# Performance work log

Measured on AMD Instinct MI355X. Metric: run time of the kernel, lower is better.

Reference implementation:

```python
import jax, jax.numpy as jnp
import numpy as np

B, C, H, D, W = 1, 32, 32, 32, 32   # batch, channels, 3D grid
M1 = M2 = M3 = 16                   # fourier modes kept per dim
KS = 3                              # spatial attention kernel size
MEM = 5                             # memory slots
EPS = 1e-5
N = H * D * W


def _gelu(x):
    return jax.nn.gelu(x, approximate=False)  # torch exact GELU


def _gn(x):
    # GroupNorm(1, C) without affine: normalize over (C,H,D,W) per sample
    mu = jnp.mean(x, axis=(1, 2, 3, 4), keepdims=True)
    var = jnp.var(x, axis=(1, 2, 3, 4), keepdims=True)
    return (x - mu) * jax.lax.rsqrt(var + EPS)


def _spectral_conv(x, wr, wi):
    # classic 3D FNO spectral conv: keep low modes (4 corner blocks in dims H,D; low block in rfft dim W)
    xf = jnp.fft.rfftn(x, axes=(2, 3, 4))                 # (B,C,H,D,W//2+1) complex64
    w = wr + 1j * wi                                      # (4,Cin,Cout,M1,M2,M3)
    of = jnp.zeros((x.shape[0], C, H, D, W // 2 + 1), xf.dtype)
    corners = [(slice(0, M1), slice(0, M2)), (slice(H - M1, H), slice(0, M2)),
               (slice(0, M1), slice(D - M2, D)), (slice(H - M1, H), slice(D - M2, D))]
    for i, (s1, s2) in enumerate(corners):
        of = of.at[:, :, s1, s2, :M3].set(
            jnp.einsum('bixyz,ioxyz->boxyz', xf[:, :, s1, s2, :M3], w[i]))
    return jnp.fft.irfftn(of, s=(H, D, W), axes=(2, 3, 4))


def _forward(x, t, prev_memory, w_spec_r, w_spec_i, norm1_g, norm1_b,
             mlp_w1, mlp_b1, mlp_w2, mlp_b2, tin_gw, tin_gb, tin_bw, tin_bb,
             q_w, q_b, k_w, k_b, v_w, v_b, mem_key, mem_value,
             gate_w, gate_b, gru_wih, gru_whh, gru_bih, gru_bhh):
    skip1 = x
    skip2 = _gelu(x)
    # spectral conv -> GroupNorm(affine) + residual -> gelu
    h = _spectral_conv(x, w_spec_r, w_spec_i)
    h = _gelu(_gn(h) * norm1_g[None, :, None, None, None]
              + norm1_b[None, :, None, None, None] + skip1)
    # pointwise Conv1d MLP over channels
    hf = h.reshape(B, C, N)
    u = _gelu(jnp.einsum('oc,bcn->bon', mlp_w1, hf) + mlp_b1[None, :, None])
    hf = jnp.einsum('oc,bcn->bon', mlp_w2, u) + mlp_b2[None, :, None]
    h = hf.reshape(B, C, H, D, W)
    # time-conditioned instance norm: gamma/beta from 1x1 conv over t (B,C)
    gamma = (jnp.einsum('oc,bc->bo', tin_gw, t) + tin_gb)[:, :, None, None, None]
    beta = (jnp.einsum('oc,bc->bo', tin_bw, t) + tin_bb)[:, :, None, None, None]
    h = gamma * _gn(h) + beta
    # ---- spatial attention with memory ----
    pad = KS // 2
    xp = jnp.pad(h, ((0, 0), (0, 0), (pad, pad), (pad, pad), (pad, pad)))
    # 3D unfold: (B,C,27,N) patches via 27 shifted views
    patches = jnp.stack([xp[:, :, i:i + H, j:j + D, l:l + W]
                         for i in range(KS) for j in range(KS) for l in range(KS)],
                        axis=2).reshape(B, C, KS ** 3, N)
    hf = h.reshape(B, C, N)
    q = jnp.einsum('oc,bcn->bon', q_w, hf) + q_b[None, :, None]              # (B,C,N)
    k_sp = jnp.einsum('oc,bcmn->bomn', k_w, patches) + k_b[None, :, None, None]
    v_sp = jnp.einsum('oc,bcmn->bomn', v_w, patches) + v_b[None, :, None, None]
    mem_k = jnp.broadcast_to(mem_key[None, :, :, None], (B, C, MEM, N))
    mem_v = jnp.broadcast_to(mem_value[None, :, :, None], (B, C, MEM, N))
    k = jnp.concatenate([mem_k, k_sp], axis=2)                               # (B,C,32,N)
    v = jnp.concatenate([mem_v, v_sp], axis=2)
    attn = jax.nn.softmax(q[:, :, None, :] * k / jnp.sqrt(jnp.float32(C)), axis=2)
    out = jnp.sum(attn * v, axis=2)                                          # (B,C,N)
    cat = jnp.concatenate([hf, out], axis=1)                                 # (B,2C,N)
    gate = jax.nn.sigmoid(jnp.einsum('oc,bcn->bon', gate_w, cat) + gate_b[None, :, None])
    out = gate * out + (1.0 - gate) * hf
    out = out.reshape(B, C, H, D, W)
    # GRUCell memory update from spatially pooled features
    m_in = jnp.mean(out, axis=(2, 3, 4))                                     # (B,C)
    gi = m_in @ gru_wih.T + gru_bih
    gh = prev_memory @ gru_whh.T + gru_bhh
    ir, iz, inn = jnp.split(gi, 3, axis=1)
    hr, hz, hn = jnp.split(gh, 3, axis=1)
    r = jax.nn.sigmoid(ir + hr)
    z = jax.nn.sigmoid(iz + hz)
    n = jnp.tanh(inn + r * hn)
    new_memory = (1.0 - z) * n + z * prev_memory                             # (B,C)
    return out + skip2, new_memory


def setup_inputs():
    key = jax.random.key(0)
    ks = jax.random.split(key, 20)
    def rn(k, shape, s):
        return jax.random.normal(k, shape, jnp.float32) * s
    spec_scale = 1.0 / (C * C)
    return dict(
        x=jax.random.normal(ks[0], (B, C, H, D, W), jnp.float32),
        t=jax.random.normal(ks[1], (B, C), jnp.float32),
        prev_memory=jnp.zeros((B, C), jnp.float32),
        w_spec_r=rn(ks[2], (4, C, C, M1, M2, M3), spec_scale),
        w_spec_i=rn(ks[3], (4, C, C, M1, M2, M3), spec_scale),
        norm1_g=jnp.ones((C,), jnp.float32),
        norm1_b=jnp.zeros((C,), jnp.float32),
        mlp_w1=rn(ks[4], (C // 2, C), 0.1), mlp_b1=jnp.zeros((C // 2,), jnp.float32),
        mlp_w2=rn(ks[5], (C, C // 2), 0.1), mlp_b2=jnp.zeros((C,), jnp.float32),
        tin_gw=rn(ks[6], (C, C), 0.1), tin_gb=jnp.ones((C,), jnp.float32),
        tin_bw=rn(ks[7], (C, C), 0.1), tin_bb=jnp.zeros((C,), jnp.float32),
        q_w=rn(ks[8], (C, C), 0.1), q_b=jnp.zeros((C,), jnp.float32),
        k_w=rn(ks[9], (C, C), 0.1), k_b=jnp.zeros((C,), jnp.float32),
        v_w=rn(ks[10], (C, C), 0.1), v_b=jnp.zeros((C,), jnp.float32),
        mem_key=jax.random.normal(ks[11], (C, MEM), jnp.float32),
        mem_value=jax.random.normal(ks[12], (C, MEM), jnp.float32),
        gate_w=rn(ks[13], (C, 2 * C), 0.1), gate_b=jnp.zeros((C,), jnp.float32),
        gru_wih=rn(ks[14], (3 * C, C), 0.1), gru_whh=rn(ks[15], (3 * C, C), 0.1),
        gru_bih=jnp.zeros((3 * C,), jnp.float32), gru_bhh=jnp.zeros((3 * C,), jnp.float32),
    )


def reference(x, t, prev_memory, w_spec_r, w_spec_i, norm1_g, norm1_b,
              mlp_w1, mlp_b1, mlp_w2, mlp_b2, tin_gw, tin_gb, tin_bw, tin_bb,
              q_w, q_b, k_w, k_b, v_w, v_b, mem_key, mem_value,
              gate_w, gate_b, gru_wih, gru_whh, gru_bih, gru_bhh):
    return _forward(x, t, prev_memory, w_spec_r, w_spec_i, norm1_g, norm1_b,
                    mlp_w1, mlp_b1, mlp_w2, mlp_b2, tin_gw, tin_gb, tin_bw, tin_bb,
                    q_w, q_b, k_w, k_b, v_w, v_b, mem_key, mem_value,
                    gate_w, gate_b, gru_wih, gru_whh, gru_bih, gru_bhh)
```

## Files before the change

### kernel.cpp

```cpp
#include <hip/hip_runtime.h>
#include <hip/hip_bf16.h>
#include <math.h>

#define NSP 32768
#define NZ 17

typedef float f4_t __attribute__((ext_vector_type(4)));

__device__ __forceinline__ float geluf(float x){
    return 0.5f * x * (1.0f + erff(x * 0.70710678118654752f));
}
__device__ __forceinline__ float sigmoidf_(float x){
    return 1.0f / (1.0f + __expf(-x));
}


__global__ void k_fwd(const float* __restrict__ x, float* __restrict__ Br, float* __restrict__ Bi){
    __shared__ float tile[32*33];
    __shared__ float ar[544], ai[544];
    __shared__ float ct[32], st[32];
    int b = blockIdx.x, t = threadIdx.x;
    if (t < 32){ float ang = 6.283185307179586477f * (float)t / 32.0f; ct[t] = cosf(ang); st[t] = sinf(ang); }
    const float* src = x + b * 1024;
    for (int j = t; j < 1024; j += 256) tile[(j & 31) * 33 + (j >> 5)] = src[j];
    __syncthreads();
    for (int idx = t; idx < 544; idx += 256){
        int d = idx / 17, z = idx - d * 17;
        float sr = 0.f, si = 0.f;
        #pragma unroll
        for (int w = 0; w < 32; ++w){
            int a = (z * w) & 31;
            float v = tile[w * 33 + d];
            sr += v * ct[a];
            si -= v * st[a];
        }
        ar[idx] = sr; ai[idx] = si;
    }
    __syncthreads();
    for (int idx = t; idx < 544; idx += 256){
        int kd = idx / 17, z = idx - kd * 17;
        float sr = 0.f, si = 0.f;
        #pragma unroll
        for (int d = 0; d < 32; ++d){
            int a = (kd * d) & 31;
            float c = ct[a], s = st[a];
            float vr = ar[d * 17 + z], vi = ai[d * 17 + z];
            sr += vr * c + vi * s;
            si += vi * c - vr * s;
        }
        Br[b * 544 + idx] = sr; Bi[b * 544 + idx] = si;
    }
}

__global__ void k_fft_h(const float* __restrict__ Br, const float* __restrict__ Bi,
                        float* __restrict__ Ar, float* __restrict__ Ai){
    __shared__ float ir[544], ii[544];
    __shared__ float ct[32], st[32];
    int b = blockIdx.x, t = threadIdx.x;
    int c = b >> 5, d = b & 31;
    if (t < 32){ float ang = 6.283185307179586477f * (float)t / 32.0f; ct[t] = cosf(ang); st[t] = sinf(ang); }
    for (int j = t; j < 544; j += 256){
        int h = j / 17, z = j - h * 17;
        int g = ((c * 32 + h) * 32 + d) * NZ + z;
        ir[j] = Br[g]; ii[j] = Bi[g];
    }
    __syncthreads();
    for (int idx = t; idx < 544; idx += 256){
        int kh = idx / 17, z = idx - kh * 17;
        float sr = 0.f, si = 0.f;
        #pragma unroll
        for (int h = 0; h < 32; ++h){
            int a = (kh * h) & 31;
            float c2 = ct[a], s2 = st[a];
            float vr = ir[h * 17 + z], vi = ii[h * 17 + z];
            sr += vr * c2 + vi * s2;
            si += vi * c2 - vr * s2;
        }
        int g = ((c * 32 + kh) * 32 + d) * NZ + z;
        Ar[g] = sr; Ai[g] = si;
    }
}

__global__ void k_modemul(const float* __restrict__ Xr, const float* __restrict__ Xi,
                          const float* __restrict__ Wr, const float* __restrict__ Wi,
                          float* __restrict__ Or, float* __restrict__ Oi){
    int b = blockIdx.x;
    int q = b & 3;
    int o = (b >> 2) & 31;
    int corner = b >> 7;
    int t = threadIdx.x;
    int m = q * 1024 + t * 4;
    int xm = m >> 8, ym = (m >> 4) & 15, zm = m & 15;
    int xg = xm + ((corner & 1) << 4);
    int y  = ym + ((corner >> 1) << 4);
    if (t < 128){
        int xl = t >> 5;
        int arr = (t >> 4) & 1;
        int yl = t & 15;
        int xgz = q * 4 + xl + ((corner & 1) << 4);
        int yz = yl + ((corner >> 1) << 4);
        int g = ((o * 32 + xgz) * 32 + yz) * NZ + 16;
        if (arr == 0) Or[g] = 0.f; else Oi[g] = 0.f;
    }
    size_t xoff = (size_t)(xg * 32 + y) * NZ + zm;
    const float* wr = Wr + (size_t)((corner * 32) * 32 + o) * 4096 + m;
    const float* wi = Wi + (size_t)((corner * 32) * 32 + o) * 4096 + m;
    float ar0=0.f, ar1=0.f, ar2=0.f, ar3=0.f;
    float ai0=0.f, ai1=0.f, ai2=0.f, ai3=0.f;
    #pragma unroll 4
    for (int i = 0; i < 32; ++i){
        f4_t w4r = __builtin_nontemporal_load((const f4_t*)(wr + (size_t)i * 131072));
        f4_t w4i = __builtin_nontemporal_load((const f4_t*)(wi + (size_t)i * 131072));
        const float* pxr = Xr + (size_t)i * 17408 + xoff;
        const float* pxi = Xi + (size_t)i * 17408 + xoff;
        float xr0 = pxr[0], xr1 = pxr[1], xr2 = pxr[2], xr3 = pxr[3];
        float xi0 = pxi[0], xi1 = pxi[1], xi2 = pxi[2], xi3 = pxi[3];
        ar0 += w4r.x * xr0 - w4i.x * xi0;  ai0 += w4r.x * xi0 + w4i.x * xr0;
        ar1 += w4r.y * xr1 - w4i.y * xi1;  ai1 += w4r.y * xi1 + w4i.y * xr1;
        ar2 += w4r.z * xr2 - w4i.z * xi2;  ai2 += w4r.z * xi2 + w4i.z * xr2;
        ar3 += w4r.w * xr3 - w4i.w * xi3;  ai3 += w4r.w * xi3 + w4i.w * xr3;
    }
    int g = ((o * 32 + xg) * 32 + y) * NZ + zm;
    Or[g + 0] = ar0; Or[g + 1] = ar1; Or[g + 2] = ar2; Or[g + 3] = ar3;
    Oi[g + 0] = ai0; Oi[g + 1] = ai1; Oi[g + 2] = ai2; Oi[g + 3] = ai3;
}

__global__ void k_ifft_h(const float* __restrict__ Br, const float* __restrict__ Bi,
                         float* __restrict__ Ar, float* __restrict__ Ai){
    __shared__ float ir[544], ii[544];
    __shared__ float ct[32], st[32];
    int b = blockIdx.x, t = threadIdx.x;
    int c = b >> 5, y = b & 31;
    if (t < 32){ float ang = 6.283185307179586477f * (float)t / 32.0f; ct[t] = cosf(ang); st[t] = sinf(ang); }
    for (int j = t; j < 544; j += 256){
        int xk = j / 17, z = j - xk * 17;
        int g = ((c * 32 + xk) * 32 + y) * NZ + z;
        ir[j] = Br[g]; ii[j] = Bi[g];
    }
    __syncthreads();
    for (int idx = t; idx < 544; idx += 256){
        int h = idx / 17, z = idx - h * 17;
        float sr = 0.f, si = 0.f;
        #pragma unroll
        for (int k = 0; k < 32; ++k){
            int a = (k * h) & 31;
            float c2 = ct[a], s2 = st[a];
            float vr = ir[k * 17 + z], vi = ii[k * 17 + z];
            sr += vr * c2 - vi * s2;
            si += vr * s2 + vi * c2;
        }
        int g = ((c * 32 + h) * 32 + y) * NZ + z;
        Ar[g] = sr; Ai[g] = si;
    }
}

__global__ void k_inv(const float* __restrict__ Ar, const float* __restrict__ Ai,
                      float* __restrict__ spec,
                      float* __restrict__ psum, float* __restrict__ psq){
    __shared__ float ir[544], ii[544];
    __shared__ float cr[544], ci[544];
    __shared__ float ct[32], st[32];
    __shared__ float ls[256], lq[256];
    int b = blockIdx.x, t = threadIdx.x;
    if (t < 32){ float ang = 6.283185307179586477f * (float)t / 32.0f; ct[t] = cosf(ang); st[t] = sinf(ang); }
    const float* pr = Ar + b * 544;
    const float* pi = Ai + b * 544;
    for (int j = t; j < 544; j += 256){ ir[j] = pr[j]; ii[j] = pi[j]; }
    __syncthreads();
    for (int idx = t; idx < 544; idx += 256){
        int d = idx / 17, z = idx - d * 17;
        float sr = 0.f, si = 0.f;
        #pragma unroll
        for (int k = 0; k < 32; ++k){
            int a = (k * d) & 31;
            float c2 = ct[a], s2 = st[a];
            float vr = ir[k * 17 + z], vi = ii[k * 17 + z];
            sr += vr * c2 - vi * s2;
            si += vr * s2 + vi * c2;
        }
        cr[idx] = sr; ci[idx] = si;
    }
    __syncthreads();
    const float inv = 1.0f / 32768.0f;
    float s_loc = 0.f, q_loc = 0.f;
    for (int idx = t; idx < 1024; idx += 256){
        int d = idx >> 5, w = idx & 31;
        float s = cr[d * 17 + 0] + ((w & 1) ? -cr[d * 17 + 16] : cr[d * 17 + 16]);
        #pragma unroll
        for (int z = 1; z < 16; ++z){
            int a = (z * w) & 31;
            s += 2.0f * (cr[d * 17 + z] * ct[a] - ci[d * 17 + z] * st[a]);
        }
        s *= inv;
        spec[b * 1024 + idx] = s;
        s_loc += s; q_loc += s * s;
    }
    ls[t] = s_loc; lq[t] = q_loc; __syncthreads();
    for (int off = 128; off > 0; off >>= 1){
        if (t < off){ ls[t] += ls[t + off]; lq[t] += lq[t + off]; }
        __syncthreads();
    }
    if (t == 0){ psum[b] = ls[0]; psq[b] = lq[0]; }
}


__global__ void k_mlp(const float* __restrict__ spec, const float* __restrict__ x,
                      const float* __restrict__ n1g, const float* __restrict__ n1b,
                      const float* __restrict__ psum, const float* __restrict__ psq,
                      const float* __restrict__ w1, const float* __restrict__ b1,
                      const float* __restrict__ w2, const float* __restrict__ b2,
                      float* __restrict__ h2,
                      float* __restrict__ psum2, float* __restrict__ psq2){
    __shared__ float W1[512], W2[512], B1[16], B2[32], GG[32], BB[32];
    __shared__ float ls[256], lq[256];
    int t = threadIdx.x;
    for (int j = t; j < 512; j += 256){ W1[j] = w1[j]; W2[j] = w2[j]; }
    if (t < 16) B1[t] = b1[t];
    if (t < 32){ B2[t] = b2[t]; GG[t] = n1g[t]; BB[t] = n1b[t]; }
    float s0 = 0.f, q0 = 0.f;
    for (int j = t; j < 1024; j += 256){ s0 += psum[j]; q0 += psq[j]; }
    ls[t] = s0; lq[t] = q0; __syncthreads();
    for (int off = 128; off > 0; off >>= 1){
        if (t < off){ ls[t] += ls[t + off]; lq[t] += lq[t + off]; }
        __syncthreads();
    }
    float mu = ls[0] * (1.0f / 1048576.0f);
    float var = lq[0] * (1.0f / 1048576.0f) - mu * mu;
    float rs = rsqrtf(var + 1e-5f);
    __syncthreads();
    int n = blockIdx.x * 256 + t;
    float hv[32];
    #pragma unroll
    for (int c = 0; c < 32; ++c){
        float v = (spec[c * NSP + n] - mu) * rs * GG[c] + BB[c] + x[c * NSP + n];
        hv[c] = geluf(v);
    }
    float u[16];
    #pragma unroll
    for (int o = 0; o < 16; ++o){
        float a = B1[o];
        #pragma unroll
        for (int c = 0; c < 32; ++c) a += W1[o * 32 + c] * hv[c];
        u[o] = geluf(a);
    }
    float s_loc = 0.f, q_loc = 0.f;
    #pragma unroll
    for (int o = 0; o < 32; ++o){
        float a = B2[o];
        #pragma unroll
        for (int c = 0; c < 16; ++c) a += W2[o * 16 + c] * u[c];
        h2[o * NSP + n] = a;
        s_loc += a; q_loc += a * a;
    }
    ls[t] = s_loc; lq[t] = q_loc; __syncthreads();
    for (int off = 128; off > 0; off >>= 1){
        if (t < off){ ls[t] += ls[t + off]; lq[t] += lq[t + off]; }
        __syncthreads();
    }
    if (t == 0){ psum2[blockIdx.x] = ls[0]; psq2[blockIdx.x] = lq[0]; }
}

__global__ void k_qkv(const float* __restrict__ h2,
                      const float* __restrict__ psum2, const float* __restrict__ psq2,
                      const float* __restrict__ tin,
                      const float* __restrict__ tgw, const float* __restrict__ tgb,
                      const float* __restrict__ tbw, const float* __restrict__ tbb,
                      const float* __restrict__ qw, const float* __restrict__ qb,
                      const float* __restrict__ kw, const float* __restrict__ vw,
                      float* __restrict__ h3, float* __restrict__ Q,
                      float* __restrict__ KH, float* __restrict__ VH){
    __shared__ float QW[1024], KW[1024], VW[1024], GA[32], BE[32], QB[32];
    __shared__ float ls[256], lq[256];
    int t = threadIdx.x;
    for (int j = t; j < 1024; j += 256){ QW[j] = qw[j]; KW[j] = kw[j]; VW[j] = vw[j]; }
    if (t < 32) QB[t] = qb[t];
    ls[t] = (t < 128) ? psum2[t] : 0.f;
    lq[t] = (t < 128) ? psq2[t] : 0.f;
    __syncthreads();
    for (int off = 128; off > 0; off >>= 1){
        if (t < off){ ls[t] += ls[t + off]; lq[t] += lq[t + off]; }
        __syncthreads();
    }
    float mu = ls[0] * (1.0f / 1048576.0f);
    float var = lq[0] * (1.0f / 1048576.0f) - mu * mu;
    float rs = rsqrtf(var + 1e-5f);
    __syncthreads();
    if (t < 64){
        int o = t & 31;
        const float* w = (t < 32) ? tgw : tbw;
        const float* bi = (t < 32) ? tgb : tbb;
        float a = bi[o];
        #pragma unroll
        for (int c = 0; c < 32; ++c) a += w[o * 32 + c] * tin[c];
        if (t < 32) GA[o] = a; else BE[o] = a;
    }
    __syncthreads();
    int n = blockIdx.x * 256 + t;
    float hv[32];
    #pragma unroll
    for (int c = 0; c < 32; ++c){
        float v = GA[c] * ((h2[c * NSP + n] - mu) * rs) + BE[c];
        hv[c] = v;
        h3[c * NSP + n] = v;
    }
    #pragma unroll
    for (int o = 0; o < 32; ++o){
        float aq = QB[o], ak = 0.f, av = 0.f;
        #pragma unroll
        for (int c = 0; c < 32; ++c){
            float v = hv[c];
            aq += QW[o * 32 + c] * v;
            ak += KW[o * 32 + c] * v;
            av += VW[o * 32 + c] * v;
        }
        Q[o * NSP + n] = aq;
        KH[o * NSP + n] = ak;
        VH[o * NSP + n] = av;
    }
}

__global__ void k_attn(const float* __restrict__ Q, const float* __restrict__ KH,
                       const float* __restrict__ VH,
                       const float* __restrict__ kb, const float* __restrict__ vb,
                       const float* __restrict__ mk, const float* __restrict__ mv,
                       float* __restrict__ out0){
    __shared__ float KL[3][1024], VL[3][1024];
    int bid = blockIdx.x;
    int swz = (bid & 7) * 128 + (bid >> 3);
    int c = swz >> 5, h_ = swz & 31;
    int t = threadIdx.x;
    #pragma unroll
    for (int p = 0; p < 3; ++p){
        int hh = h_ - 1 + p;
        if ((unsigned)hh < 32u){
            const float* sk = KH + (c * 32 + hh) * 1024;
            const float* sv = VH + (c * 32 + hh) * 1024;
            for (int j = t; j < 1024; j += 256){ KL[p][j] = sk[j]; VL[p][j] = sv[j]; }
        }
    }
    float kbc = kb[c], vbc = vb[c];
    float mkv[5], mvv[5];
    #pragma unroll
    for (int j = 0; j < 5; ++j){ mkv[j] = mk[c * 5 + j]; mvv[j] = mv[c * 5 + j]; }
    float qv[4];
    #pragma unroll
    for (int i = 0; i < 4; ++i) qv[i] = Q[c * NSP + h_ * 1024 + i * 256 + t];
    __syncthreads();
    const float scale = 0.17677669529663688f;
    #pragma unroll
    for (int i = 0; i < 4; ++i){
        int nl = i * 256 + t;
        int d_ = nl >> 5, w_ = nl & 31;
        float q = qv[i];
        float s = 0.f, acc = 0.f;
        #pragma unroll
        for (int j = 0; j < 5; ++j){
            float e = __expf(q * mkv[j] * scale);
            s += e; acc += e * mvv[j];
        }
        int oob = 0;
        #pragma unroll
        for (int p = 0; p < 3; ++p){
            int hh = h_ - 1 + p;
            if ((unsigned)hh >= 32u){ oob += 9; continue; }
            #pragma unroll
            for (int dj = -1; dj <= 1; ++dj){
                int dd = d_ + dj;
                if ((unsigned)dd >= 32u){ oob += 3; continue; }
                int rb = dd * 32;
                #pragma unroll
                for (int dl = -1; dl <= 1; ++dl){
                    int ww = w_ + dl;
                    if ((unsigned)ww < 32u){
                        float k = kbc + KL[p][rb + ww];
                        float v = vbc + VL[p][rb + ww];
                        float e = __expf(q * k * scale);
                        s += e; acc += e * v;
                    } else oob++;
                }
            }
        }
        float eb = __expf(q * kbc * scale);
        s += (float)oob * eb; acc += (float)oob * eb * vbc;
        out0[c * NSP + h_ * 1024 + nl] = acc / s;
    }
}

__global__ void k_gate(const float* __restrict__ h3, const float* __restrict__ out0,
                       const float* __restrict__ x,
                       const float* __restrict__ gw, const float* __restrict__ gb,
                       float* __restrict__ outp, float* __restrict__ mpart){
    __shared__ float GW[2048];
    __shared__ float FT[32 * 264];
    __shared__ float PS[256];
    int t = threadIdx.x;
    for (int j = t; j < 2048; j += 256) GW[j] = gw[j];
    int n = blockIdx.x * 256 + t;
    float hv[32], ov[32];
    #pragma unroll
    for (int c = 0; c < 32; ++c){ hv[c] = h3[c * NSP + n]; ov[c] = out0[c * NSP + n]; }
    __syncthreads();
    #pragma unroll
    for (int c = 0; c < 32; ++c){
        float g = gb[c];
        #pragma unroll
        for (int cc = 0; cc < 32; ++cc){
            g += GW[c * 64 + cc] * hv[cc] + GW[c * 64 + 32 + cc] * ov[cc];
        }
        g = sigmoidf_(g);
        float fin = g * ov[c] + (1.0f - g) * hv[c];
        FT[c * 264 + t] = fin;
        outp[c * NSP + n] = fin + geluf(x[c * NSP + n]);
    }
    __syncthreads();
    {
        int c8 = t >> 3, seg = t & 7;
        float s = 0.f;
        #pragma unroll
        for (int j = 0; j < 32; ++j) s += FT[c8 * 264 + seg * 32 + j];
        PS[t] = s;
    }
    __syncthreads();
    if (t < 32){
        float s = 0.f;
        #pragma unroll
        for (int j = 0; j < 8; ++j) s += PS[t * 8 + j];
        mpart[t * 128 + blockIdx.x] = s;
    }
}

__global__ void k_gru(const float* __restrict__ mpart, const float* __restrict__ pm,
                      const float* __restrict__ wih, const float* __restrict__ whh,
                      const float* __restrict__ bih, const float* __restrict__ bhh,
                      float* __restrict__ outp){
    __shared__ float PS[256];
    __shared__ float m_in[32], gi[96], gh[96];
    int t = threadIdx.x;
    {
        int c = t >> 3, seg = t & 7;
        float s = 0.f;
        #pragma unroll
        for (int j = 0; j < 16; ++j) s += mpart[c * 128 + seg * 16 + j];
        PS[t] = s;
    }
    __syncthreads();
    if (t < 32){
        float a = 0.f;
        #pragma unroll
        for (int j = 0; j < 8; ++j) a += PS[t * 8 + j];
        m_in[t] = a * (1.0f / 32768.0f);
    }
    __syncthreads();
    if (t < 96){
        float a = bih[t], b2 = bhh[t];
        #pragma unroll
        for (int cc = 0; cc < 32; ++cc){
            a += wih[t * 32 + cc] * m_in[cc];
            b2 += whh[t * 32 + cc] * pm[cc];
        }
        gi[t] = a; gh[t] = b2;
    }
    __syncthreads();
    if (t < 32){
        float r = sigmoidf_(gi[t] + gh[t]);
        float z = sigmoidf_(gi[32 + t] + gh[32 + t]);
        float nn = tanhf(gi[64 + t] + r * gh[64 + t]);
        float nm = (1.0f - z) * nn + z * pm[t];
        outp[1048576 + t] = nm;
    }
}

extern "C" void kernel_launch(void* const* d_in, const int* in_sizes, int n_in,
                              void* d_out, int out_size, void* d_ws, size_t ws_size,
                              hipStream_t stream){
    const float* x   = (const float*)d_in[0];
    const float* tin = (const float*)d_in[1];
    const float* pm  = (const float*)d_in[2];
    const float* wsr = (const float*)d_in[3];
    const float* wsi = (const float*)d_in[4];
    const float* n1g = (const float*)d_in[5];
    const float* n1b = (const float*)d_in[6];
    const float* mw1 = (const float*)d_in[7];
    const float* mb1 = (const float*)d_in[8];
    const float* mw2 = (const float*)d_in[9];
    const float* mb2 = (const float*)d_in[10];
    const float* tgw = (const float*)d_in[11];
    const float* tgb = (const float*)d_in[12];
    const float* tbw = (const float*)d_in[13];
    const float* tbb = (const float*)d_in[14];
    const float* qw  = (const float*)d_in[15];
    const float* qb  = (const float*)d_in[16];
    const float* kw  = (const float*)d_in[17];
    const float* kb  = (const float*)d_in[18];
    const float* vw  = (const float*)d_in[19];
    const float* vb  = (const float*)d_in[20];
    const float* mk  = (const float*)d_in[21];
    const float* mv  = (const float*)d_in[22];
    const float* gw  = (const float*)d_in[23];
    const float* gb  = (const float*)d_in[24];
    const float* wih = (const float*)d_in[25];
    const float* whh = (const float*)d_in[26];
    const float* bih = (const float*)d_in[27];
    const float* bhh = (const float*)d_in[28];

    float* ws = (float*)d_ws;
    float* Ar    = ws + 0;
    float* Ai    = ws + 557056;
    float* Br    = ws + 1114112;
    float* Bi    = ws + 1671168;
    float* spec  = ws + 2228224;
    float* h1    = ws + 3276800;
    float* h2    = ws + 4325376;
    float* h3    = ws + 5373952;
    float* psum  = ws + 6422784;
    float* psq   = ws + 6423808;
    float* psum2 = ws + 6424832;
    float* psq2  = ws + 6425856;
    float* Qb    = Br;
    float* KHb   = spec;
    float* VHb   = h1;
    float* out0  = Ar;
    float* mpart = h2;

    float* outp = (float*)d_out;

    k_fwd    <<<1024, 256, 0, stream>>>(x, Br, Bi);
    k_fft_h  <<<1024, 256, 0, stream>>>(Br, Bi, Ar, Ai);
    k_modemul<<<512, 256, 0, stream>>>(Ar, Ai, wsr, wsi, Br, Bi);
    k_ifft_h <<<1024, 256, 0, stream>>>(Br, Bi, Ar, Ai);
    k_inv    <<<1024, 256, 0, stream>>>(Ar, Ai, spec, psum, psq);
    k_mlp    <<<128, 256, 0, stream>>>(spec, x, n1g, n1b, psum, psq, mw1, mb1, mw2, mb2, h2, psum2, psq2);
    k_qkv    <<<128, 256, 0, stream>>>(h2, psum2, psq2, tin, tgw, tgb, tbw, tbb, qw, qb, kw, vw, h3, Qb, KHb, VHb);
    k_attn   <<<1024, 256, 0, stream>>>(Qb, KHb, VHb, kb, vb, mk, mv, out0);
    k_gate   <<<128, 256, 0, stream>>>(h3, out0, x, gw, gb, outp, mpart);
    k_gru    <<<1, 256, 0, stream>>>(mpart, pm, wih, whh, bih, bhh, outp);
}
```

Baseline: 199.4 us.

## Fuse all stages into one cooperative persistent kernel with grid syncs

Replaces the ten separate kernel launches with a single cooperative kernel of 512 blocks that loops over work items and uses grid.sync between stages. The stages and the shared-memory buffers are unchanged, with the shared memory aliased through a union. The goal is to remove launch overhead and inter-kernel gaps. In exchange, the stages that use only 128 blocks leave most of the grid idle, the 512-block grid may limit occupancy, and each grid sync adds a barrier cost. If the cooperative launch fails, the code falls back to the original sequence of launches.

```diff
diff --git a/kernel.cpp b/kernel.cpp
--- a/kernel.cpp
+++ b/kernel.cpp
@@ -1,6 +1,9 @@
 #include <hip/hip_runtime.h>
 #include <hip/hip_bf16.h>
+#include <hip/hip_cooperative_groups.h>
 #include <math.h>
+
+namespace cg = cooperative_groups;
 
 #define NSP 32768
 #define NZ 17
@@ -12,6 +15,446 @@
 }
 __device__ __forceinline__ float sigmoidf_(float x){
     return 1.0f / (1.0f + __expf(-x));
+}
+__device__ __forceinline__ float wavesum(float v){
+    #pragma unroll
+    for (int off = 32; off > 0; off >>= 1) v += __shfl_down(v, off, 64);
+    return v;
+}
+
+struct MegaParams {
+    const float *x, *tin, *pm;
+    const float *wsr, *wsi;
+    const float *n1g, *n1b;
+    const float *mw1, *mb1, *mw2, *mb2;
+    const float *tgw, *tgb, *tbw, *tbb;
+    const float *qw, *qb, *kw, *kb, *vw, *vb;
+    const float *mk, *mv, *gw, *gb;
+    const float *wih, *whh, *bih, *bhh;
+    float *Ar, *Ai, *Br, *Bi, *spec, *h1, *h2, *h3;
+    float *psum, *psq, *psum2, *psq2;
+    float *outp;
+};
+
+union SMem {
+    struct { float tile[32*33]; float ar[544], ai[544]; } fwd;
+    struct { float ir[544], ii[544]; } ffth;
+    struct { float ir[544], ii[544], cr[544], ci[544]; } inv;
+    struct { float W1[512], W2[512], B1[16], B2[32], GG[32], BB[32]; } mlp;
+    struct { float QW[1024], KW[1024], VW[1024], GA[32], BE[32], QB[32]; } qkv;
+    struct { float KL[3][1024], VL[3][1024]; } attn;
+    struct { float GW[2048]; float WS[4][32]; } gate;
+    struct { float PS[256]; float m_in[32], gi[96], gh[96]; } gru;
+};
+
+__global__ void __launch_bounds__(256, 4) k_mega(MegaParams P){
+    cg::grid_group grid = cg::this_grid();
+    __shared__ SMem sm;
+    __shared__ float ls[256], lq[256];
+    __shared__ float ct[32], st[32];
+    int b0 = blockIdx.x, t = threadIdx.x;
+    if (t < 32){ float ang = 6.283185307179586477f * (float)t / 32.0f; ct[t] = cosf(ang); st[t] = sinf(ang); }
+    __syncthreads();
+
+    for (int b = b0; b < 1024; b += 512){
+        const float* src = P.x + b * 1024;
+        for (int j = t; j < 1024; j += 256) sm.fwd.tile[(j & 31) * 33 + (j >> 5)] = src[j];
+        __syncthreads();
+        for (int idx = t; idx < 544; idx += 256){
+            int d = idx / 17, z = idx - d * 17;
+            float sr = 0.f, si = 0.f;
+            #pragma unroll
+            for (int w = 0; w < 32; ++w){
+                int a = (z * w) & 31;
+                float v = sm.fwd.tile[w * 33 + d];
+                sr += v * ct[a];
+                si -= v * st[a];
+            }
+            sm.fwd.ar[idx] = sr; sm.fwd.ai[idx] = si;
+        }
+        __syncthreads();
+        for (int idx = t; idx < 544; idx += 256){
+            int kd = idx / 17, z = idx - kd * 17;
+            float sr = 0.f, si = 0.f;
+            #pragma unroll
+            for (int d = 0; d < 32; ++d){
+                int a = (kd * d) & 31;
+                float c = ct[a], s = st[a];
+                float vr = sm.fwd.ar[d * 17 + z], vi = sm.fwd.ai[d * 17 + z];
+                sr += vr * c + vi * s;
+                si += vi * c - vr * s;
+            }
+            P.Br[b * 544 + idx] = sr; P.Bi[b * 544 + idx] = si;
+        }
+        __syncthreads();
+    }
+    grid.sync();
+
+    for (int b = b0; b < 1024; b += 512){
+        int c = b >> 5, d = b & 31;
+        for (int j = t; j < 544; j += 256){
+            int h = j / 17, z = j - h * 17;
+            int g = ((c * 32 + h) * 32 + d) * NZ + z;
+            sm.ffth.ir[j] = P.Br[g]; sm.ffth.ii[j] = P.Bi[g];
+        }
+        __syncthreads();
+        for (int idx = t; idx < 544; idx += 256){
+            int kh = idx / 17, z = idx - kh * 17;
+            float sr = 0.f, si = 0.f;
+            #pragma unroll
+            for (int h = 0; h < 32; ++h){
+                int a = (kh * h) & 31;
+                float c2 = ct[a], s2 = st[a];
+                float vr = sm.ffth.ir[h * 17 + z], vi = sm.ffth.ii[h * 17 + z];
+                sr += vr * c2 + vi * s2;
+                si += vi * c2 - vr * s2;
+            }
+            int g = ((c * 32 + kh) * 32 + d) * NZ + z;
+            P.Ar[g] = sr; P.Ai[g] = si;
+        }
+        __syncthreads();
+    }
+    grid.sync();
+
+    {
+        int b = b0;
+        int q = b & 3;
+        int o = (b >> 2) & 31;
+        int corner = b >> 7;
+        int m = q * 1024 + t * 4;
+        int xm = m >> 8, ym = (m >> 4) & 15, zm = m & 15;
+        int xg = xm + ((corner & 1) << 4);
+        int y  = ym + ((corner >> 1) << 4);
+        if (t < 128){
+            int xl = t >> 5;
+            int arr = (t >> 4) & 1;
+            int yl = t & 15;
+            int xgz = q * 4 + xl + ((corner & 1) << 4);
+            int yz = yl + ((corner >> 1) << 4);
+            int g = ((o * 32 + xgz) * 32 + yz) * NZ + 16;
+            if (arr == 0) P.Br[g] = 0.f; else P.Bi[g] = 0.f;
+        }
+        size_t xoff = (size_t)(xg * 32 + y) * NZ + zm;
+        const float* wr = P.wsr + (size_t)((corner * 32) * 32 + o) * 4096 + m;
+        const float* wi = P.wsi + (size_t)((corner * 32) * 32 + o) * 4096 + m;
+        float ar0=0.f, ar1=0.f, ar2=0.f, ar3=0.f;
+        float ai0=0.f, ai1=0.f, ai2=0.f, ai3=0.f;
+        #pragma unroll 4
+        for (int i = 0; i < 32; ++i){
+            f4_t w4r = __builtin_nontemporal_load((const f4_t*)(wr + (size_t)i * 131072));
+            f4_t w4i = __builtin_nontemporal_load((const f4_t*)(wi + (size_t)i * 131072));
+            const float* pxr = P.Ar + (size_t)i * 17408 + xoff;
+            const float* pxi = P.Ai + (size_t)i * 17408 + xoff;
+            float xr0 = pxr[0], xr1 = pxr[1], xr2 = pxr[2], xr3 = pxr[3];
+            float xi0 = pxi[0], xi1 = pxi[1], xi2 = pxi[2], xi3 = pxi[3];
+            ar0 += w4r.x * xr0 - w4i.x * xi0;  ai0 += w4r.x * xi0 + w4i.x * xr0;
+            ar1 += w4r.y * xr1 - w4i.y * xi1;  ai1 += w4r.y * xi1 + w4i.y * xr1;
+            ar2 += w4r.z * xr2 - w4i.z * xi2;  ai2 += w4r.z * xi2 + w4i.z * xr2;
+            ar3 += w4r.w * xr3 - w4i.w * xi3;  ai3 += w4r.w * xi3 + w4i.w * xr3;
+        }
+        int g = ((o * 32 + xg) * 32 + y) * NZ + zm;
+        P.Br[g + 0] = ar0; P.Br[g + 1] = ar1; P.Br[g + 2] = ar2; P.Br[g + 3] = ar3;
+        P.Bi[g + 0] = ai0; P.Bi[g + 1] = ai1; P.Bi[g + 2] = ai2; P.Bi[g + 3] = ai3;
+    }
+    grid.sync();
+
+    for (int b = b0; b < 1024; b += 512){
+        int c = b >> 5, y = b & 31;
+        for (int j = t; j < 544; j += 256){
+            int xk = j / 17, z = j - xk * 17;
+            int g = ((c * 32 + xk) * 32 + y) * NZ + z;
+            sm.ffth.ir[j] = P.Br[g]; sm.ffth.ii[j] = P.Bi[g];
+        }
+        __syncthreads();
+        for (int idx = t; idx < 544; idx += 256){
+            int h = idx / 17, z = idx - h * 17;
+            float sr = 0.f, si = 0.f;
+            #pragma unroll
+            for (int k = 0; k < 32; ++k){
+                int a = (k * h) & 31;
+                float c2 = ct[a], s2 = st[a];
+                float vr = sm.ffth.ir[k * 17 + z], vi = sm.ffth.ii[k * 17 + z];
+                sr += vr * c2 - vi * s2;
+                si += vr * s2 + vi * c2;
+            }
+            int g = ((c * 32 + h) * 32 + y) * NZ + z;
+            P.Ar[g] = sr; P.Ai[g] = si;
+        }
+        __syncthreads();
+    }
+    grid.sync();
+
+    for (int b = b0; b < 1024; b += 512){
+        const float* pr = P.Ar + b * 544;
+        const float* pi = P.Ai + b * 544;
+        for (int j = t; j < 544; j += 256){ sm.inv.ir[j] = pr[j]; sm.inv.ii[j] = pi[j]; }
+        __syncthreads();
+        for (int idx = t; idx < 544; idx += 256){
+            int d = idx / 17, z = idx - d * 17;
+            float sr = 0.f, si = 0.f;
+            #pragma unroll
+            for (int k = 0; k < 32; ++k){
+                int a = (k * d) & 31;
+                float c2 = ct[a], s2 = st[a];
+                float vr = sm.inv.ir[k * 17 + z], vi = sm.inv.ii[k * 17 + z];
+                sr += vr * c2 - vi * s2;
+                si += vr * s2 + vi * c2;
+            }
+            sm.inv.cr[idx] = sr; sm.inv.ci[idx] = si;
+        }
+        __syncthreads();
+        const float inv = 1.0f / 32768.0f;
+        float s_loc = 0.f, q_loc = 0.f;
+        for (int idx = t; idx < 1024; idx += 256){
+            int d = idx >> 5, w = idx & 31;
+            float s = sm.inv.cr[d * 17 + 0] + ((w & 1) ? -sm.inv.cr[d * 17 + 16] : sm.inv.cr[d * 17 + 16]);
+            #pragma unroll
+            for (int z = 1; z < 16; ++z){
+                int a = (z * w) & 31;
+                s += 2.0f * (sm.inv.cr[d * 17 + z] * ct[a] - sm.inv.ci[d * 17 + z] * st[a]);
+            }
+            s *= inv;
+            P.spec[b * 1024 + idx] = s;
+            s_loc += s; q_loc += s * s;
+        }
+        ls[t] = s_loc; lq[t] = q_loc; __syncthreads();
+        for (int off = 128; off > 0; off >>= 1){
+            if (t < off){ ls[t] += ls[t + off]; lq[t] += lq[t + off]; }
+            __syncthreads();
+        }
+        if (t == 0){ P.psum[b] = ls[0]; P.psq[b] = lq[0]; }
+        __syncthreads();
+    }
+    grid.sync();
+
+    if (b0 < 128){
+        int b = b0;
+        for (int j = t; j < 512; j += 256){ sm.mlp.W1[j] = P.mw1[j]; sm.mlp.W2[j] = P.mw2[j]; }
+        if (t < 16) sm.mlp.B1[t] = P.mb1[t];
+        if (t < 32){ sm.mlp.B2[t] = P.mb2[t]; sm.mlp.GG[t] = P.n1g[t]; sm.mlp.BB[t] = P.n1b[t]; }
+        float s0 = 0.f, q0 = 0.f;
+        for (int j = t; j < 1024; j += 256){ s0 += P.psum[j]; q0 += P.psq[j]; }
+        ls[t] = s0; lq[t] = q0; __syncthreads();
+        for (int off = 128; off > 0; off >>= 1){
+            if (t < off){ ls[t] += ls[t + off]; lq[t] += lq[t + off]; }
+            __syncthreads();
+        }
+        float mu = ls[0] * (1.0f / 1048576.0f);
+        float var = lq[0] * (1.0f / 1048576.0f) - mu * mu;
+        float rs = rsqrtf(var + 1e-5f);
+        __syncthreads();
+        int n = b * 256 + t;
+        float hv[32];
+        #pragma unroll
+        for (int c = 0; c < 32; ++c){
+            float v = (P.spec[c * NSP + n] - mu) * rs * sm.mlp.GG[c] + sm.mlp.BB[c] + P.x[c * NSP + n];
+            hv[c] = geluf(v);
+        }
+        float u[16];
+        #pragma unroll
+        for (int o = 0; o < 16; ++o){
+            float a = sm.mlp.B1[o];
+            #pragma unroll
+            for (int c = 0; c < 32; ++c) a += sm.mlp.W1[o * 32 + c] * hv[c];
+            u[o] = geluf(a);
+        }
+        float s_loc = 0.f, q_loc = 0.f;
+        #pragma unroll
+        for (int o = 0; o < 32; ++o){
+            float a = sm.mlp.B2[o];
+            #pragma unroll
+            for (int c = 0; c < 16; ++c) a += sm.mlp.W2[o * 16 + c] * u[c];
+            P.h2[o * NSP + n] = a;
+            s_loc += a; q_loc += a * a;
+        }
+        ls[t] = s_loc; lq[t] = q_loc; __syncthreads();
+        for (int off = 128; off > 0; off >>= 1){
+            if (t < off){ ls[t] += ls[t + off]; lq[t] += lq[t + off]; }
+            __syncthreads();
+        }
+        if (t == 0){ P.psum2[b] = ls[0]; P.psq2[b] = lq[0]; }
+    }
+    grid.sync();
+
+    if (b0 < 128){
+        int b = b0;
+        for (int j = t; j < 1024; j += 256){ sm.qkv.QW[j] = P.qw[j]; sm.qkv.KW[j] = P.kw[j]; sm.qkv.VW[j] = P.vw[j]; }
+        if (t < 32) sm.qkv.QB[t] = P.qb[t];
+        ls[t] = (t < 128) ? P.psum2[t] : 0.f;
+        lq[t] = (t < 128) ? P.psq2[t] : 0.f;
+        __syncthreads();
+        for (int off = 128; off > 0; off >>= 1){
+            if (t < off){ ls[t] += ls[t + off]; lq[t] += lq[t + off]; }
+            __syncthreads();
+        }
+        float mu = ls[0] * (1.0f / 1048576.0f);
+        float var = lq[0] * (1.0f / 1048576.0f) - mu * mu;
+        float rs = rsqrtf(var + 1e-5f);
+        __syncthreads();
+        if (t < 64){
+            int o = t & 31;
+            const float* w = (t < 32) ? P.tgw : P.tbw;
+            const float* bi = (t < 32) ? P.tgb : P.tbb;
+            float a = bi[o];
+            #pragma unroll
+            for (int c = 0; c < 32; ++c) a += w[o * 32 + c] * P.tin[c];
+            if (t < 32) sm.qkv.GA[o] = a; else sm.qkv.BE[o] = a;
+        }
+        __syncthreads();
+        int n = b * 256 + t;
+        float hv[32];
+        #pragma unroll
+        for (int c = 0; c < 32; ++c){
+            float v = sm.qkv.GA[c] * ((P.h2[c * NSP + n] - mu) * rs) + sm.qkv.BE[c];
+            hv[c] = v;
+            P.h3[c * NSP + n] = v;
+        }
+        #pragma unroll
+        for (int o = 0; o < 32; ++o){
+            float aq = sm.qkv.QB[o], ak = 0.f, av = 0.f;
+            #pragma unroll
+            for (int c = 0; c < 32; ++c){
+                float v = hv[c];
+                aq += sm.qkv.QW[o * 32 + c] * v;
+                ak += sm.qkv.KW[o * 32 + c] * v;
+                av += sm.qkv.VW[o * 32 + c] * v;
+            }
+            P.Br[o * NSP + n] = aq;
+            P.spec[o * NSP + n] = ak;
+            P.h1[o * NSP + n] = av;
+        }
+    }
+    grid.sync();
+
+    for (int b = b0; b < 1024; b += 512){
+        int swz = (b & 7) * 128 + (b >> 3);
+        int c = swz >> 5, h_ = swz & 31;
+        const float* Q  = P.Br;
+        const float* KH = P.spec;
+        const float* VH = P.h1;
+        #pragma unroll
+        for (int p = 0; p < 3; ++p){
+            int hh = h_ - 1 + p;
+            if ((unsigned)hh < 32u){
+                const float* sk = KH + (c * 32 + hh) * 1024;
+                const float* sv = VH + (c * 32 + hh) * 1024;
+                for (int j = t; j < 1024; j += 256){ sm.attn.KL[p][j] = sk[j]; sm.attn.VL[p][j] = sv[j]; }
+            }
+        }
+        float kbc = P.kb[c], vbc = P.vb[c];
+        float mkv[5], mvv[5];
+        #pragma unroll
+        for (int j = 0; j < 5; ++j){ mkv[j] = P.mk[c * 5 + j]; mvv[j] = P.mv[c * 5 + j]; }
+        float qv[4];
+        #pragma unroll
+        for (int i = 0; i < 4; ++i) qv[i] = Q[c * NSP + h_ * 1024 + i * 256 + t];
+        __syncthreads();
+        const float scale = 0.17677669529663688f;
+        #pragma unroll
+        for (int i = 0; i < 4; ++i){
+            int nl = i * 256 + t;
+            int d_ = nl >> 5, w_ = nl & 31;
+            float q = qv[i];
+            float s = 0.f, acc = 0.f;
+            #pragma unroll
+            for (int j = 0; j < 5; ++j){
+                float e = __expf(q * mkv[j] * scale);
+                s += e; acc += e * mvv[j];
+            }
+            int oob = 0;
+            #pragma unroll
+            for (int p = 0; p < 3; ++p){
+                int hh = h_ - 1 + p;
+                if ((unsigned)hh >= 32u){ oob += 9; continue; }
+                #pragma unroll
+                for (int dj = -1; dj <= 1; ++dj){
+                    int dd = d_ + dj;
+                    if ((unsigned)dd >= 32u){ oob += 3; continue; }
+                    int rb = dd * 32;
+                    #pragma unroll
+                    for (int dl = -1; dl <= 1; ++dl){
+                        int ww = w_ + dl;
+                        if ((unsigned)ww < 32u){
+                            float k = kbc + sm.attn.KL[p][rb + ww];
+                            float v = vbc + sm.attn.VL[p][rb + ww];
+                            float e = __expf(q * k * scale);
+                            s += e; acc += e * v;
+                        } else oob++;
+                    }
+                }
+            }
+            float eb = __expf(q * kbc * scale);
+            s += (float)oob * eb; acc += (float)oob * eb * vbc;
+            P.Ar[c * NSP + h_ * 1024 + nl] = acc / s;
+        }
+        __syncthreads();
+    }
+    grid.sync();
+
+    if (b0 < 128){
+        int b = b0;
+        for (int j = t; j < 2048; j += 256) sm.gate.GW[j] = P.gw[j];
+        __syncthreads();
+        int n = b * 256 + t;
+        int lane = t & 63, wv = t >> 6;
+        float hv[32], ov[32];
+        #pragma unroll
+        for (int c = 0; c < 32; ++c){ hv[c] = P.h3[c * NSP + n]; ov[c] = P.Ar[c * NSP + n]; }
+        #pragma unroll
+        for (int c = 0; c < 32; ++c){
+            float g = P.gb[c];
+            #pragma unroll
+            for (int cc = 0; cc < 32; ++cc){
+                g += sm.gate.GW[c * 64 + cc] * hv[cc] + sm.gate.GW[c * 64 + 32 + cc] * ov[cc];
+            }
+            g = sigmoidf_(g);
+            float fin = g * ov[c] + (1.0f - g) * hv[c];
+            P.outp[c * NSP + n] = fin + geluf(P.x[c * NSP + n]);
+            float ssum = wavesum(fin);
+            if (lane == 0) sm.gate.WS[wv][c] = ssum;
+        }
+        __syncthreads();
+        if (t < 32){
+            float s = sm.gate.WS[0][t] + sm.gate.WS[1][t] + sm.gate.WS[2][t] + sm.gate.WS[3][t];
+            P.h2[t * 128 + b] = s;
+        }
+    }
+    grid.sync();
+
+    if (b0 == 0){
+        {
+            int c = t >> 3, seg = t & 7;
+            float s = 0.f;
+            #pragma unroll
+            for (int j = 0; j < 16; ++j) s += P.h2[c * 128 + seg * 16 + j];
+            sm.gru.PS[t] = s;
+        }
+        __syncthreads();
+        if (t < 32){
+            float a = 0.f;
+            #pragma unroll
+            for (int j = 0; j < 8; ++j) a += sm.gru.PS[t * 8 + j];
+            sm.gru.m_in[t] = a * (1.0f / 32768.0f);
+        }
+        __syncthreads();
+        if (t < 96){
+            float a = P.bih[t], b2 = P.bhh[t];
+            #pragma unroll
+            for (int cc = 0; cc < 32; ++cc){
+                a += P.wih[t * 32 + cc] * sm.gru.m_in[cc];
+                b2 += P.whh[t * 32 + cc] * P.pm[cc];
+            }
+            sm.gru.gi[t] = a; sm.gru.gh[t] = b2;
+        }
+        __syncthreads();
+        if (t < 32){
+            float r = sigmoidf_(sm.gru.gi[t] + sm.gru.gh[t]);
+            float z = sigmoidf_(sm.gru.gi[32 + t] + sm.gru.gh[32 + t]);
+            float nn = tanhf(sm.gru.gi[64 + t] + r * sm.gru.gh[64 + t]);
+            float nm = (1.0f - z) * nn + z * P.pm[t];
+            P.outp[1048576 + t] = nm;
+        }
+    }
 }
 
 
@@ -203,7 +646,6 @@
     if (t == 0){ psum[b] = ls[0]; psq[b] = lq[0]; }
 }
 
-
 __global__ void k_mlp(const float* __restrict__ spec, const float* __restrict__ x,
                       const float* __restrict__ n1g, const float* __restrict__ n1b,
                       const float* __restrict__ psum, const float* __restrict__ psq,
@@ -473,65 +915,63 @@
 extern "C" void kernel_launch(void* const* d_in, const int* in_sizes, int n_in,
                               void* d_out, int out_size, void* d_ws, size_t ws_size,
                               hipStream_t stream){
-    const float* x   = (const float*)d_in[0];
-    const float* tin = (const float*)d_in[1];
-    const float* pm  = (const float*)d_in[2];
-    const float* wsr = (const float*)d_in[3];
-    const float* wsi = (const float*)d_in[4];
-    const float* n1g = (const float*)d_in[5];
-    const float* n1b = (const float*)d_in[6];
-    const float* mw1 = (const float*)d_in[7];
-    const float* mb1 = (const float*)d_in[8];
-    const float* mw2 = (const float*)d_in[9];
-    const float* mb2 = (const float*)d_in[10];
-    const float* tgw = (const float*)d_in[11];
-    const float* tgb = (const float*)d_in[12];
-    const float* tbw = (const float*)d_in[13];
-    const float* tbb = (const float*)d_in[14];
-    const float* qw  = (const float*)d_in[15];
-    const float* qb  = (const float*)d_in[16];
-    const float* kw  = (const float*)d_in[17];
-    const float* kb  = (const float*)d_in[18];
-    const float* vw  = (const float*)d_in[19];
-    const float* vb  = (const float*)d_in[20];
-    const float* mk  = (const float*)d_in[21];
-    const float* mv  = (const float*)d_in[22];
-    const float* gw  = (const float*)d_in[23];
-    const float* gb  = (const float*)d_in[24];
-    const float* wih = (const float*)d_in[25];
-    const float* whh = (const float*)d_in[26];
-    const float* bih = (const float*)d_in[27];
-    const float* bhh = (const float*)d_in[28];
-
     float* ws = (float*)d_ws;
-    float* Ar    = ws + 0;
-    float* Ai    = ws + 557056;
-    float* Br    = ws + 1114112;
-    float* Bi    = ws + 1671168;
-    float* spec  = ws + 2228224;
-    float* h1    = ws + 3276800;
-    float* h2    = ws + 4325376;
-    float* h3    = ws + 5373952;
-    float* psum  = ws + 6422784;
-    float* psq   = ws + 6423808;
-    float* psum2 = ws + 6424832;
-    float* psq2  = ws + 6425856;
-    float* Qb    = Br;
-    float* KHb   = spec;
-    float* VHb   = h1;
-    float* out0  = Ar;
-    float* mpart = h2;
-
-    float* outp = (float*)d_out;
-
-    k_fwd    <<<1024, 256, 0, stream>>>(x, Br, Bi);
-    k_fft_h  <<<1024, 256, 0, stream>>>(Br, Bi, Ar, Ai);
-    k_modemul<<<512, 256, 0, stream>>>(Ar, Ai, wsr, wsi, Br, Bi);
-    k_ifft_h <<<1024, 256, 0, stream>>>(Br, Bi, Ar, Ai);
-    k_inv    <<<1024, 256, 0, stream>>>(Ar, Ai, spec, psum, psq);
-    k_mlp    <<<128, 256, 0, stream>>>(spec, x, n1g, n1b, psum, psq, mw1, mb1, mw2, mb2, h2, psum2, psq2);
-    k_qkv    <<<128, 256, 0, stream>>>(h2, psum2, psq2, tin, tgw, tgb, tbw, tbb, qw, qb, kw, vw, h3, Qb, KHb, VHb);
-    k_attn   <<<1024, 256, 0, stream>>>(Qb, KHb, VHb, kb, vb, mk, mv, out0);
-    k_gate   <<<128, 256, 0, stream>>>(h3, out0, x, gw, gb, outp, mpart);
-    k_gru    <<<1, 256, 0, stream>>>(mpart, pm, wih, whh, bih, bhh, outp);
-}
+    MegaParams P;
+    P.x   = (const float*)d_in[0];
+    P.tin = (const float*)d_in[1];
+    P.pm  = (const float*)d_in[2];
+    P.wsr = (const float*)d_in[3];
+    P.wsi = (const float*)d_in[4];
+    P.n1g = (const float*)d_in[5];
+    P.n1b = (const float*)d_in[6];
+    P.mw1 = (const float*)d_in[7];
+    P.mb1 = (const float*)d_in[8];
+    P.mw2 = (const float*)d_in[9];
+    P.mb2 = (const float*)d_in[10];
+    P.tgw = (const float*)d_in[11];
+    P.tgb = (const float*)d_in[12];
+    P.tbw = (const float*)d_in[13];
+    P.tbb = (const float*)d_in[14];
+    P.qw  = (const float*)d_in[15];
+    P.qb  = (const float*)d_in[16];
+    P.kw  = (const float*)d_in[17];
+    P.kb  = (const float*)d_in[18];
+    P.vw  = (const float*)d_in[19];
+    P.vb  = (const float*)d_in[20];
+    P.mk  = (const float*)d_in[21];
+    P.mv  = (const float*)d_in[22];
+    P.gw  = (const float*)d_in[23];
+    P.gb  = (const float*)d_in[24];
+    P.wih = (const float*)d_in[25];
+    P.whh = (const float*)d_in[26];
+    P.bih = (const float*)d_in[27];
+    P.bhh = (const float*)d_in[28];
+    P.Ar    = ws + 0;
+    P.Ai    = ws + 557056;
+    P.Br    = ws + 1114112;
+    P.Bi    = ws + 1671168;
+    P.spec  = ws + 2228224;
+    P.h1    = ws + 3276800;
+    P.h2    = ws + 4325376;
+    P.h3    = ws + 5373952;
+    P.psum  = ws + 6422784;
+    P.psq   = ws + 6423808;
+    P.psum2 = ws + 6424832;
+    P.psq2  = ws + 6425856;
+    P.outp  = (float*)d_out;
+
+    void* args[] = { &P };
+    hipError_t err = hipLaunchCooperativeKernel((const void*)k_mega, dim3(512), dim3(256), args, 0, stream);
+    if (err != hipSuccess){
+        k_fwd    <<<1024, 256, 0, stream>>>(P.x, P.Br, P.Bi);
+        k_fft_h  <<<1024, 256, 0, stream>>>(P.Br, P.Bi, P.Ar, P.Ai);
+        k_modemul<<<512, 256, 0, stream>>>(P.Ar, P.Ai, P.wsr, P.wsi, P.Br, P.Bi);
+        k_ifft_h <<<1024, 256, 0, stream>>>(P.Br, P.Bi, P.Ar, P.Ai);
+        k_inv    <<<1024, 256, 0, stream>>>(P.Ar, P.Ai, P.spec, P.psum, P.psq);
+        k_mlp    <<<128, 256, 0, stream>>>(P.spec, P.x, P.n1g, P.n1b, P.psum, P.psq, P.mw1, P.mb1, P.mw2, P.mb2, P.h2, P.psum2, P.psq2);
+        k_qkv    <<<128, 256, 0, stream>>>(P.h2, P.psum2, P.psq2, P.tin, P.tgw, P.tgb, P.tbw, P.tbb, P.qw, P.qb, P.kw, P.vw, P.h3, P.Br, P.spec, P.h1);
+        k_attn   <<<1024, 256, 0, stream>>>(P.Br, P.spec, P.h1, P.kb, P.vb, P.mk, P.mv, P.Ar);
+        k_gate   <<<128, 256, 0, stream>>>(P.h3, P.Ar, P.x, P.gw, P.gb, P.outp, P.h2);
+        k_gru    <<<1, 256, 0, stream>>>(P.h2, P.pm, P.wih, P.whh, P.bih, P.bhh, P.outp);
+    }
+}
```

After: 761.4 us. 282% more time.

## Drop unused Nyquist z-mode and relayout spectral intermediates for coalesced access

Applied to the files above, without the earlier changes.

Only the 16 low rfft modes in z are kept by the spectral weights, so the forward FFT stages now compute 16 instead of 17 z-frequencies and the inverse drops the zeroed Nyquist term. Intermediate buffers are relaid out: the first stage writes h-contiguous data so the H-FFT reads contiguously with padded shared memory, and the mode multiply writes in (o,y,x,z) order so the inverse H stage reads a contiguous block. This removes the zeroing writes and strided gathers, at the cost of coupling host buffer strides to the new layouts, which are not visible here.

```diff
diff --git a/kernel.cpp b/kernel.cpp
--- a/kernel.cpp
+++ b/kernel.cpp
@@ -3,7 +3,6 @@
 #include <math.h>
 
 #define NSP 32768
-#define NZ 17
 
 typedef float f4_t __attribute__((ext_vector_type(4)));
 
@@ -15,17 +14,17 @@
 }
 
 
-__global__ void k_fwd(const float* __restrict__ x, float* __restrict__ Br, float* __restrict__ Bi){
+__global__ void k_fwd(const float* __restrict__ x, float* __restrict__ T1r, float* __restrict__ T1i){
     __shared__ float tile[32*33];
-    __shared__ float ar[544], ai[544];
+    __shared__ float ar[512], ai[512];
     __shared__ float ct[32], st[32];
     int b = blockIdx.x, t = threadIdx.x;
     if (t < 32){ float ang = 6.283185307179586477f * (float)t / 32.0f; ct[t] = cosf(ang); st[t] = sinf(ang); }
     const float* src = x + b * 1024;
     for (int j = t; j < 1024; j += 256) tile[(j & 31) * 33 + (j >> 5)] = src[j];
     __syncthreads();
-    for (int idx = t; idx < 544; idx += 256){
-        int d = idx / 17, z = idx - d * 17;
+    for (int idx = t; idx < 512; idx += 256){
+        int d = idx >> 4, z = idx & 15;
         float sr = 0.f, si = 0.f;
         #pragma unroll
         for (int w = 0; w < 32; ++w){
@@ -37,46 +36,48 @@
         ar[idx] = sr; ai[idx] = si;
     }
     __syncthreads();
-    for (int idx = t; idx < 544; idx += 256){
-        int kd = idx / 17, z = idx - kd * 17;
+    int c = b >> 5, h = b & 31;
+    for (int idx = t; idx < 512; idx += 256){
+        int kd = idx >> 4, z = idx & 15;
         float sr = 0.f, si = 0.f;
         #pragma unroll
         for (int d = 0; d < 32; ++d){
             int a = (kd * d) & 31;
-            float c = ct[a], s = st[a];
-            float vr = ar[d * 17 + z], vi = ai[d * 17 + z];
-            sr += vr * c + vi * s;
-            si += vi * c - vr * s;
-        }
-        Br[b * 544 + idx] = sr; Bi[b * 544 + idx] = si;
-    }
-}
-
-__global__ void k_fft_h(const float* __restrict__ Br, const float* __restrict__ Bi,
+            float c0 = ct[a], s0 = st[a];
+            float vr = ar[d * 16 + z], vi = ai[d * 16 + z];
+            sr += vr * c0 + vi * s0;
+            si += vi * c0 - vr * s0;
+        }
+        int g = (c * 512 + idx) * 32 + h;
+        T1r[g] = sr; T1i[g] = si;
+    }
+}
+
+__global__ void k_fft_h(const float* __restrict__ T1r, const float* __restrict__ T1i,
                         float* __restrict__ Ar, float* __restrict__ Ai){
-    __shared__ float ir[544], ii[544];
+    __shared__ float ir[16*33], ii[16*33];
     __shared__ float ct[32], st[32];
     int b = blockIdx.x, t = threadIdx.x;
-    int c = b >> 5, d = b & 31;
+    int c = b >> 5, kd = b & 31;
     if (t < 32){ float ang = 6.283185307179586477f * (float)t / 32.0f; ct[t] = cosf(ang); st[t] = sinf(ang); }
-    for (int j = t; j < 544; j += 256){
-        int h = j / 17, z = j - h * 17;
-        int g = ((c * 32 + h) * 32 + d) * NZ + z;
-        ir[j] = Br[g]; ii[j] = Bi[g];
-    }
-    __syncthreads();
-    for (int idx = t; idx < 544; idx += 256){
-        int kh = idx / 17, z = idx - kh * 17;
+    for (int j = t; j < 512; j += 256){
+        int z = j >> 5, h = j & 31;
+        ir[z * 33 + h] = T1r[b * 512 + j];
+        ii[z * 33 + h] = T1i[b * 512 + j];
+    }
+    __syncthreads();
+    for (int idx = t; idx < 512; idx += 256){
+        int kh = idx >> 4, z = idx & 15;
         float sr = 0.f, si = 0.f;
         #pragma unroll
         for (int h = 0; h < 32; ++h){
             int a = (kh * h) & 31;
             float c2 = ct[a], s2 = st[a];
-            float vr = ir[h * 17 + z], vi = ii[h * 17 + z];
+            float vr = ir[z * 33 + h], vi = ii[z * 33 + h];
             sr += vr * c2 + vi * s2;
             si += vi * c2 - vr * s2;
         }
-        int g = ((c * 32 + kh) * 32 + d) * NZ + z;
+        int g = ((c * 32 + kh) * 32 + kd) * 16 + z;
         Ar[g] = sr; Ai[g] = si;
     }
 }
@@ -93,16 +94,7 @@
     int xm = m >> 8, ym = (m >> 4) & 15, zm = m & 15;
     int xg = xm + ((corner & 1) << 4);
     int y  = ym + ((corner >> 1) << 4);
-    if (t < 128){
-        int xl = t >> 5;
-        int arr = (t >> 4) & 1;
-        int yl = t & 15;
-        int xgz = q * 4 + xl + ((corner & 1) << 4);
-        int yz = yl + ((corner >> 1) << 4);
-        int g = ((o * 32 + xgz) * 32 + yz) * NZ + 16;
-        if (arr == 0) Or[g] = 0.f; else Oi[g] = 0.f;
-    }
-    size_t xoff = (size_t)(xg * 32 + y) * NZ + zm;
+    size_t xoff = (size_t)((xg * 32 + y) * 16 + zm);
     const float* wr = Wr + (size_t)((corner * 32) * 32 + o) * 4096 + m;
     const float* wi = Wi + (size_t)((corner * 32) * 32 + o) * 4096 + m;
     float ar0=0.f, ar1=0.f, ar2=0.f, ar3=0.f;
@@ -111,8 +103,8 @@
     for (int i = 0; i < 32; ++i){
         f4_t w4r = __builtin_nontemporal_load((const f4_t*)(wr + (size_t)i * 131072));
         f4_t w4i = __builtin_nontemporal_load((const f4_t*)(wi + (size_t)i * 131072));
-        const float* pxr = Xr + (size_t)i * 17408 + xoff;
-        const float* pxi = Xi + (size_t)i * 17408 + xoff;
+        const float* pxr = Xr + (size_t)i * 16384 + xoff;
+        const float* pxi = Xi + (size_t)i * 16384 + xoff;
         float xr0 = pxr[0], xr1 = pxr[1], xr2 = pxr[2], xr3 = pxr[3];
         float xi0 = pxi[0], xi1 = pxi[1], xi2 = pxi[2], xi3 = pxi[3];
         ar0 += w4r.x * xr0 - w4i.x * xi0;  ai0 += w4r.x * xi0 + w4i.x * xr0;
@@ -120,36 +112,32 @@
         ar2 += w4r.z * xr2 - w4i.z * xi2;  ai2 += w4r.z * xi2 + w4i.z * xr2;
         ar3 += w4r.w * xr3 - w4i.w * xi3;  ai3 += w4r.w * xi3 + w4i.w * xr3;
     }
-    int g = ((o * 32 + xg) * 32 + y) * NZ + zm;
+    int g = ((o * 32 + y) * 32 + xg) * 16 + zm;
     Or[g + 0] = ar0; Or[g + 1] = ar1; Or[g + 2] = ar2; Or[g + 3] = ar3;
     Oi[g + 0] = ai0; Oi[g + 1] = ai1; Oi[g + 2] = ai2; Oi[g + 3] = ai3;
 }
 
 __global__ void k_ifft_h(const float* __restrict__ Br, const float* __restrict__ Bi,
                          float* __restrict__ Ar, float* __restrict__ Ai){
-    __shared__ float ir[544], ii[544];
+    __shared__ float ir[512], ii[512];
     __shared__ float ct[32], st[32];
     int b = blockIdx.x, t = threadIdx.x;
-    int c = b >> 5, y = b & 31;
+    int o = b >> 5, y = b & 31;
     if (t < 32){ float ang = 6.283185307179586477f * (float)t / 32.0f; ct[t] = cosf(ang); st[t] = sinf(ang); }
-    for (int j = t; j < 544; j += 256){
-        int xk = j / 17, z = j - xk * 17;
-        int g = ((c * 32 + xk) * 32 + y) * NZ + z;
-        ir[j] = Br[g]; ii[j] = Bi[g];
-    }
-    __syncthreads();
-    for (int idx = t; idx < 544; idx += 256){
-        int h = idx / 17, z = idx - h * 17;
+    for (int j = t; j < 512; j += 256){ ir[j] = Br[b * 512 + j]; ii[j] = Bi[b * 512 + j]; }
+    __syncthreads();
+    for (int idx = t; idx < 512; idx += 256){
+        int h = idx >> 4, z = idx & 15;
         float sr = 0.f, si = 0.f;
         #pragma unroll
         for (int k = 0; k < 32; ++k){
             int a = (k * h) & 31;
             float c2 = ct[a], s2 = st[a];
-            float vr = ir[k * 17 + z], vi = ii[k * 17 + z];
+            float vr = ir[k * 16 + z], vi = ii[k * 16 + z];
             sr += vr * c2 - vi * s2;
             si += vr * s2 + vi * c2;
         }
-        int g = ((c * 32 + h) * 32 + y) * NZ + z;
+        int g = ((o * 32 + h) * 32 + y) * 16 + z;
         Ar[g] = sr; Ai[g] = si;
     }
 }
@@ -157,24 +145,22 @@
 __global__ void k_inv(const float* __restrict__ Ar, const float* __restrict__ Ai,
                       float* __restrict__ spec,
                       float* __restrict__ psum, float* __restrict__ psq){
-    __shared__ float ir[544], ii[544];
-    __shared__ float cr[544], ci[544];
+    __shared__ float ir[512], ii[512];
+    __shared__ float cr[512], ci[512];
     __shared__ float ct[32], st[32];
     __shared__ float ls[256], lq[256];
     int b = blockIdx.x, t = threadIdx.x;
     if (t < 32){ float ang = 6.283185307179586477f * (float)t / 32.0f; ct[t] = cosf(ang); st[t] = sinf(ang); }
-    const float* pr = Ar + b * 544;
-    const float* pi = Ai + b * 544;
-    for (int j = t; j < 544; j += 256){ ir[j] = pr[j]; ii[j] = pi[j]; }
-    __syncthreads();
-    for (int idx = t; idx < 544; idx += 256){
-        int d = idx / 17, z = idx - d * 17;
+    for (int j = t; j < 512; j += 256){ ir[j] = Ar[b * 512 + j]; ii[j] = Ai[b * 512 + j]; }
+    __syncthreads();
+    for (int idx = t; idx < 512; idx += 256){
+        int d = idx >> 4, z = idx & 15;
         float sr = 0.f, si = 0.f;
         #pragma unroll
         for (int k = 0; k < 32; ++k){
             int a = (k * d) & 31;
             float c2 = ct[a], s2 = st[a];
-            float vr = ir[k * 17 + z], vi = ii[k * 17 + z];
+            float vr = ir[k * 16 + z], vi = ii[k * 16 + z];
             sr += vr * c2 - vi * s2;
             si += vr * s2 + vi * c2;
         }
@@ -185,11 +171,11 @@
     float s_loc = 0.f, q_loc = 0.f;
     for (int idx = t; idx < 1024; idx += 256){
         int d = idx >> 5, w = idx & 31;
-        float s = cr[d * 17 + 0] + ((w & 1) ? -cr[d * 17 + 16] : cr[d * 17 + 16]);
+        float s = cr[d * 16 + 0];
         #pragma unroll
         for (int z = 1; z < 16; ++z){
             int a = (z * w) & 31;
-            s += 2.0f * (cr[d * 17 + z] * ct[a] - ci[d * 17 + z] * st[a]);
+            s += 2.0f * (cr[d * 16 + z] * ct[a] - ci[d * 16 + z] * st[a]);
         }
         s *= inv;
         spec[b * 1024 + idx] = s;
```

Result: faster. 188.3 us (-5.6%).
